# Optimization experiments

Hardware: AMD Instinct MI355X
Metric: run time of the kernel (lower is better)

Reference implementation:

```python
import math
import jax, jax.numpy as jnp
import numpy as np

H, N2, B, L = 256, 32, 8, 4096
DT_MIN, DT_MAX = 1e-3, 1e-1

def setup_inputs() -> dict:
    key = jax.random.key(0)
    ks = jax.random.split(key, 6)
    u = jax.random.normal(ks[0], (B, H, L), dtype=jnp.float32)
    # log_dt uniform in [log(dt_min), log(dt_max)] as in S4DKernel.__init__
    log_dt = jax.random.uniform(ks[1], (H,), dtype=jnp.float32) * (
        math.log(DT_MAX) - math.log(DT_MIN)) + math.log(DT_MIN)
    C = jax.random.normal(ks[2], (H, N2, 2), dtype=jnp.float32)  # view_as_real of complex C
    log_A_real = jnp.log(0.5 * jnp.ones((H, N2), dtype=jnp.float32))
    A_imag = math.pi * jnp.broadcast_to(jnp.arange(N2, dtype=jnp.float32), (H, N2))
    D = jax.random.normal(ks[3], (H,), dtype=jnp.float32)
    W = jax.random.normal(ks[4], (2 * H, H), dtype=jnp.float32) / math.sqrt(H)
    b = jax.random.normal(ks[5], (2 * H,), dtype=jnp.float32) * 0.01
    return {"u": u, "log_dt": log_dt, "C": C, "log_A_real": log_A_real,
            "A_imag": A_imag, "D": D, "W": W, "b": b}

def reference(u, log_dt, C, log_A_real, A_imag, D, W, b):
    # ---- S4DKernel: generate convolution kernel k (H, L) ----
    Lk = u.shape[-1]
    dt = jnp.exp(log_dt)                                  # (H,)
    Cc = C[..., 0] + 1j * C[..., 1]                       # (H, N2) complex
    A = -jnp.exp(log_A_real) + 1j * A_imag                # (H, N2) complex
    dtA = A * dt[:, None]                                 # (H, N2)
    # Vandermonde: exp(dtA * l) for l in [0, L)  -> (H, N2, L) complex
    K = jnp.exp(dtA[:, :, None] * jnp.arange(Lk, dtype=jnp.float32))
    Ct = Cc * (jnp.exp(dtA) - 1.0) / A                    # (H, N2)
    k = 2.0 * jnp.einsum('hn,hnl->hl', Ct, K).real        # (H, L) float32
    # ---- FFT long convolution ----
    n = 2 * Lk
    k_f = jnp.fft.rfft(k, n=n)                            # (H, n//2+1)
    u_f = jnp.fft.rfft(u, n=n)                            # (B, H, n//2+1)
    y = jnp.fft.irfft(u_f * k_f, n=n)[..., :Lk]           # (B, H, L)
    y = y + u * D[:, None]                                # skip connection
    y = jax.nn.gelu(y, approximate=False)                 # nn.GELU (exact)
    # ---- output 1x1 conv (H -> 2H) + GLU over channel dim ----
    z = jnp.einsum('oh,bhl->bol', W, y) + b[None, :, None]  # (B, 2H, L)
    a, g = jnp.split(z, 2, axis=1)
    return a * jax.nn.sigmoid(g)                          # (B, H, L)
```

## Files before the change

### kernel.cpp

```cpp
#include <hip/hip_runtime.h>
#include <math.h>

#define H 256
#define N2 32
#define Bsz 8
#define Lseq 4096
#define BH (Bsz*H)
#define NCH 32
#define LC (Lseq/NCH)
#define HN (H*N2)

#define S_OFF  0
#define Y_OFF  (S_OFF + BH*NCH*N2*2)
#define WB_OFF (Y_OFF + (BH*Lseq/2))
#define KB_OFF (WB_OFF + (512*256/2))
#define EB_OFF (KB_OFF + (H*128/2))
#define VB_OFF (EB_OFF + (H*128*64/2))

typedef __attribute__((ext_vector_type(8))) short bf16x8;
typedef __attribute__((ext_vector_type(8))) unsigned short u16x8;
typedef __attribute__((ext_vector_type(4))) float f32x4;

__device__ __forceinline__ unsigned short f2bf(float x) {
  union { float f; unsigned int u; } v; v.f = x;
  unsigned int r = v.u + 0x7fffu + ((v.u >> 16) & 1u);
  return (unsigned short)(r >> 16);
}
__device__ __forceinline__ unsigned int packbf(float lo, float hi) {
  return (unsigned int)f2bf(lo) | ((unsigned int)f2bf(hi) << 16);
}

__global__ __launch_bounds__(128) void k_prep(const float* __restrict__ log_dt,
                                              const float* __restrict__ C,
                                              const float* __restrict__ lar,
                                              const float* __restrict__ aim,
                                              const float* __restrict__ W,
                                              unsigned short* __restrict__ Wb,
                                              unsigned short* __restrict__ kb,
                                              unsigned short* __restrict__ Eb,
                                              unsigned short* __restrict__ Vb) {
  int h = blockIdx.x;
  int j = threadIdx.x;
  {
    int i = h * 128 + j;
    float4 v = *(const float4*)&W[i * 4];
    uint2 p; p.x = packbf(v.x, v.y); p.y = packbf(v.z, v.w);
    *(uint2*)&Wb[i * 4] = p;
  }
  float dt = expf(log_dt[h]);
  float kacc = 0.f;
  unsigned short* Erow = Eb + (h * 128 + j) * 64;
  for (int n = 0; n < 32; n++) {
    int hn = (h << 5) + n;
    float Ar = -expf(lar[hn]), Ai = aim[hn];
    float dAr = Ar * dt, dAi = Ai * dt;
    float er = expf(dAr), sw, cw;
    sincosf(dAi, &sw, &cw);
    float wr = er * cw, wi = er * sw;
    float emr = wr - 1.f, emi = wi;
    float inv = 1.f / (Ar * Ar + Ai * Ai);
    float qr = (emr * Ar + emi * Ai) * inv;
    float qi = (emi * Ar - emr * Ai) * inv;
    float Cr = C[2 * hn], Ci = C[2 * hn + 1];
    float c2r = 2.f * (Cr * qr - Ci * qi);
    float c2i = 2.f * (Cr * qi + Ci * qr);
    float ej = expf(dAr * (float)j), sj, cj;
    sincosf(dAi * (float)j, &sj, &cj);
    kacc = fmaf(c2r, ej * cj, fmaf(-c2i, ej * sj, kacc));
    float e1 = expf(dAr * (float)(j + 1)), s1, c1;
    sincosf(dAi * (float)(j + 1), &s1, &c1);
    float w1r = e1 * c1, w1i = e1 * s1;
    Erow[2 * n]     = f2bf(c2r * w1r - c2i * w1i);
    Erow[2 * n + 1] = f2bf(-(c2r * w1i + c2i * w1r));
    float ev = expf(dAr * (float)(127 - j)), sv, cv;
    sincosf(dAi * (float)(127 - j), &sv, &cv);
    Vb[(h * 64 + 2 * n) * 128 + j]     = f2bf(ev * cv);
    Vb[(h * 64 + 2 * n + 1) * 128 + j] = f2bf(ev * sv);
  }
  kb[h * 128 + j] = f2bf(kacc);
}

__global__ __launch_bounds__(256) void k_state(const float* __restrict__ u,
                                               const unsigned short* __restrict__ Vb,
                                               float* __restrict__ S) {
  __shared__ unsigned short Ul[64][136];
  __shared__ unsigned short Bl[64][136];
  int h   = blockIdx.x;
  int mq  = blockIdx.y;
  int tid = threadIdx.x;
  int wv = tid >> 6, lane = tid & 63;
  int n16 = lane & 15, quad = lane >> 4;
  int m0 = wv * 16;
  f32x4 acc[4] = {};
#pragma unroll
  for (int i = 0; i < 8; i++) {
    int e = tid + i * 256;
    int r = e >> 5, c4 = e & 31;
    int b = mq * 2 + (r >> 5), c = r & 31;
    float4 v = *(const float4*)&u[((b * 256 + h) * 4096 + c * 128 + c4 * 4)];
    *(unsigned int*)&Ul[r][c4 * 4]     = packbf(v.x, v.y);
    *(unsigned int*)&Ul[r][c4 * 4 + 2] = packbf(v.z, v.w);
  }
#pragma unroll
  for (int i = 0; i < 4; i++) {
    int e = tid + i * 256;
    int p = e >> 4, s8 = e & 15;
    *(u16x8*)&Bl[p][s8 * 8] = *(const u16x8*)&Vb[(h * 64 + p) * 128 + s8 * 8];
  }
  __syncthreads();
#pragma unroll
  for (int ks = 0; ks < 128; ks += 32) {
    int kc = ks + quad * 8;
    bf16x8 af = *(const bf16x8*)&Ul[m0 + n16][kc];
#pragma unroll
    for (int nt = 0; nt < 4; nt++) {
      bf16x8 bf = *(const bf16x8*)&Bl[nt * 16 + n16][kc];
      acc[nt] = __builtin_amdgcn_mfma_f32_16x16x32_bf16(af, bf, acc[nt], 0, 0, 0);
    }
  }
#pragma unroll
  for (int reg = 0; reg < 4; reg++) {
    int m = m0 + quad * 4 + reg;
    int b = mq * 2 + (m >> 5), c = m & 31;
#pragma unroll
    for (int nt = 0; nt < 4; nt++) {
      int p = nt * 16 + n16;
      S[((b * 256 + h) * 32 + c) * 64 + p] = acc[nt][reg];
    }
  }
}

__global__ void k_prefix(const float* __restrict__ log_dt, const float* __restrict__ lar,
                         const float* __restrict__ aim, float* __restrict__ S) {
  int t = blockIdx.x * blockDim.x + threadIdx.x;
  if (t >= BH * N2) return;
  int n = t & 31, bh = t >> 5;
  int h = bh & (H - 1);
  int hn = (h << 5) + n;
  float dt  = expf(log_dt[h]);
  float dAr = -expf(lar[hn]) * dt, dAi = aim[hn] * dt;
  float eL = expf(dAr * (float)LC), sL, cL;
  sincosf(dAi * (float)LC, &sL, &cL);
  float wLr = eL * cL, wLi = eL * sL;
  float fr = 0.f, fi = 0.f;
  for (int c = 0; c < NCH; c++) {
    int si = (((bh * NCH + c) << 5) + n) << 1;
    float sr = S[si], s1 = S[si + 1];
    S[si] = fr; S[si + 1] = fi;
    float nr = fmaf(wLr, fr, fmaf(-wLi, fi, sr));
    float ni = fmaf(wLr, fi, fmaf(wLi, fr, s1));
    fr = nr; fi = ni;
  }
}

__global__ __launch_bounds__(256) void k_emit(const float* __restrict__ u,
                                              const float* __restrict__ S,
                                              const unsigned short* __restrict__ kb,
                                              const unsigned short* __restrict__ Eb,
                                              const float* __restrict__ Dp,
                                              unsigned short* __restrict__ yb) {
  __shared__ unsigned short Ul[64][72];
  __shared__ unsigned short Bl[128][72];
  __shared__ unsigned short kbuf[128];
  int h   = blockIdx.x;
  int mq  = blockIdx.y;
  int tid = threadIdx.x;
  int wv = tid >> 6, lane = tid & 63;
  int n16 = lane & 15, quad = lane >> 4;
  int m0 = wv * 16;
  f32x4 acc[8] = {};

  if (tid < 128) kbuf[tid] = kb[h * 128 + tid];

  for (int ks = 0; ks < 128; ks += 64) {
    __syncthreads();
#pragma unroll
    for (int i = 0; i < 4; i++) {
      int e = tid + i * 256;
      int r = e >> 4, c4 = e & 15;
      int b = mq * 2 + (r >> 5), c = r & 31;
      const float* up = u + ((b * 256 + h) * 4096 + c * 128 + ks + c4 * 4);
      float4 v = *(const float4*)up;
      *(unsigned int*)&Ul[r][c4 * 4]     = packbf(v.x, v.y);
      *(unsigned int*)&Ul[r][c4 * 4 + 2] = packbf(v.z, v.w);
    }
#pragma unroll
    for (int i = 0; i < 32; i++) {
      int e = tid + i * 256;
      int jj = e >> 6, m = e & 63;
      int d = jj - ks - m;
      Bl[jj][m] = (d >= 0) ? kbuf[d] : (unsigned short)0;
    }
    __syncthreads();
#pragma unroll
    for (int ks2 = 0; ks2 < 64; ks2 += 32) {
      int kc = ks2 + quad * 8;
      bf16x8 af = *(const bf16x8*)&Ul[m0 + n16][kc];
#pragma unroll
      for (int nt = 0; nt < 8; nt++) {
        bf16x8 bf = *(const bf16x8*)&Bl[nt * 16 + n16][kc];
        acc[nt] = __builtin_amdgcn_mfma_f32_16x16x32_bf16(af, bf, acc[nt], 0, 0, 0);
      }
    }
  }

  __syncthreads();
#pragma unroll
  for (int i = 0; i < 4; i++) {
    int e = tid + i * 256;
    int r = e >> 4, c4 = e & 15;
    int b = mq * 2 + (r >> 5), c = r & 31;
    const float* sp = S + ((b * 256 + h) * 32 + c) * 64 + c4 * 4;
    float4 v = *(const float4*)sp;
    *(unsigned int*)&Ul[r][c4 * 4]     = packbf(v.x, v.y);
    *(unsigned int*)&Ul[r][c4 * 4 + 2] = packbf(v.z, v.w);
  }
#pragma unroll
  for (int i = 0; i < 4; i++) {
    int e = tid + i * 256;
    int jj = e >> 3, p8 = e & 7;
    *(u16x8*)&Bl[jj][p8 * 8] = *(const u16x8*)&Eb[(h * 128 + jj) * 64 + p8 * 8];
  }
  __syncthreads();
#pragma unroll
  for (int ks2 = 0; ks2 < 64; ks2 += 32) {
    int kc = ks2 + quad * 8;
    bf16x8 af = *(const bf16x8*)&Ul[m0 + n16][kc];
#pragma unroll
    for (int nt = 0; nt < 8; nt++) {
      bf16x8 bf = *(const bf16x8*)&Bl[nt * 16 + n16][kc];
      acc[nt] = __builtin_amdgcn_mfma_f32_16x16x32_bf16(af, bf, acc[nt], 0, 0, 0);
    }
  }

  float Dh = Dp[h];
#pragma unroll
  for (int reg = 0; reg < 4; reg++) {
    int m = m0 + quad * 4 + reg;
    int b = mq * 2 + (m >> 5), c = m & 31;
    int base = (b * 256 + h) * 4096 + c * 128;
#pragma unroll
    for (int nt = 0; nt < 8; nt++) {
      int j = nt * 16 + n16;
      float uv = u[base + j];
      float v  = fmaf(Dh, uv, acc[nt][reg]);
      float ge = 0.5f * v * (1.0f + erff(v * 0.70710678118654752f));
      yb[base + j] = f2bf(ge);
    }
  }
}

__global__ __launch_bounds__(256) void k_gemm(const unsigned short* __restrict__ yb,
                                              const unsigned short* __restrict__ Wb,
                                              const float* __restrict__ bias,
                                              float* __restrict__ out) {
  __shared__ unsigned short Ws[128][72];
  __shared__ unsigned short Ys[128][72];
  int tid  = threadIdx.x;
  int l0   = blockIdx.x * 128;
  int o0   = blockIdx.y * 64;
  int bb   = blockIdx.z;
  int wave = tid >> 6;
  int lane = tid & 63;
  int wo   = wave & 1;
  int wl   = wave >> 1;
  int n    = lane & 15;
  int quad = lane >> 4;

  f32x4 acc_a[2][4] = {};
  f32x4 acc_g[2][4] = {};

  for (int kk = 0; kk < H; kk += 64) {
#pragma unroll
    for (int i = 0; i < 4; i++) {
      int e = tid + i * 256;
      int r = e >> 3, s = e & 7;
      int gr = (r < 64) ? (o0 + r) : (192 + o0 + r);
      *(u16x8*)&Ws[r][s * 8] = *(const u16x8*)&Wb[gr * 256 + kk + s * 8];
    }
    {
      int kcol = tid & 63;
      int lg0  = tid >> 6;
      const unsigned short* yrow = yb + (bb * 256 + kk + kcol) * 4096 + l0;
#pragma unroll
      for (int i = 0; i < 4; i++) {
        int l8 = (lg0 * 4 + i) * 8;
        u16x8 v = *(const u16x8*)&yrow[l8];
#pragma unroll
        for (int jj = 0; jj < 8; jj++)
          Ys[l8 + jj][kcol] = v[jj];
      }
    }
    __syncthreads();
#pragma unroll
    for (int ks = 0; ks < 64; ks += 32) {
      int kc = ks + quad * 8;
      bf16x8 af_a[2], af_g[2], bfr[4];
#pragma unroll
      for (int mt = 0; mt < 2; mt++) {
        af_a[mt] = *(const bf16x8*)&Ws[wo * 32 + mt * 16 + n][kc];
        af_g[mt] = *(const bf16x8*)&Ws[64 + wo * 32 + mt * 16 + n][kc];
      }
#pragma unroll
      for (int lt = 0; lt < 4; lt++)
        bfr[lt] = *(const bf16x8*)&Ys[wl * 64 + lt * 16 + n][kc];
#pragma unroll
      for (int mt = 0; mt < 2; mt++)
#pragma unroll
        for (int lt = 0; lt < 4; lt++) {
          acc_a[mt][lt] = __builtin_amdgcn_mfma_f32_16x16x32_bf16(af_a[mt], bfr[lt], acc_a[mt][lt], 0, 0, 0);
          acc_g[mt][lt] = __builtin_amdgcn_mfma_f32_16x16x32_bf16(af_g[mt], bfr[lt], acc_g[mt][lt], 0, 0, 0);
        }
    }
    __syncthreads();
  }
#pragma unroll
  for (int mt = 0; mt < 2; mt++) {
    int ob = o0 + wo * 32 + mt * 16 + quad * 4;
#pragma unroll
    for (int reg = 0; reg < 4; reg++) {
      int op = ob + reg;
      float ba = bias[op], bg = bias[H + op];
      float* orow = &out[(bb * H + op) * Lseq + l0 + wl * 64 + n];
#pragma unroll
      for (int lt = 0; lt < 4; lt++) {
        float a = acc_a[mt][lt][reg] + ba;
        float g = acc_g[mt][lt][reg] + bg;
        orow[lt * 16] = a / (1.0f + expf(-g));
      }
    }
  }
}

extern "C" void kernel_launch(void* const* d_in, const int* in_sizes, int n_in,
                              void* d_out, int out_size, void* d_ws, size_t ws_size,
                              hipStream_t stream) {
  const float* u      = (const float*)d_in[0];
  const float* log_dt = (const float*)d_in[1];
  const float* C      = (const float*)d_in[2];
  const float* lar    = (const float*)d_in[3];
  const float* aim    = (const float*)d_in[4];
  const float* Dp     = (const float*)d_in[5];
  const float* W      = (const float*)d_in[6];
  const float* bias   = (const float*)d_in[7];
  float* out = (float*)d_out;
  float* ws  = (float*)d_ws;
  float* S   = ws + S_OFF;
  unsigned short* yb  = (unsigned short*)(ws + Y_OFF);
  unsigned short* Wb  = (unsigned short*)(ws + WB_OFF);
  unsigned short* kbg = (unsigned short*)(ws + KB_OFF);
  unsigned short* Ebg = (unsigned short*)(ws + EB_OFF);
  unsigned short* Vbg = (unsigned short*)(ws + VB_OFF);

  hipLaunchKernelGGL(k_prep,   dim3(H), dim3(128), 0, stream, log_dt, C, lar, aim, W, Wb, kbg, Ebg, Vbg);
  hipLaunchKernelGGL(k_state,  dim3(H, 4), dim3(256), 0, stream, u, Vbg, S);
  hipLaunchKernelGGL(k_prefix, dim3(BH * N2 / 256), dim3(256), 0, stream, log_dt, lar, aim, S);
  hipLaunchKernelGGL(k_emit,   dim3(H, 4), dim3(256), 0, stream, u, S, kbg, Ebg, Dp, yb);
  hipLaunchKernelGGL(k_gemm,   dim3(Lseq / 128, H / 64, Bsz), dim3(256), 0, stream, yb, Wb, bias, out);
}
```

Before: 174.8 us.

## Precompute Toeplitz kernel tiles in prep and fuse emit into single K=192 pass

The 128x128 lower-triangular Toeplitz block of the convolution kernel is now built once per channel in k_prep and stored in the workspace, instead of being rebuilt in shared memory by every k_emit block. k_emit loads the full u chunk, the chunk states and the Toeplitz/E tiles into one shared buffer and runs a single MFMA loop over K=192, removing two barrier phases. The skip term now reads the bf16 u from shared memory instead of re-reading fp32 u from global, which slightly lowers precision. In exchange the workspace grows by an H*128*128 bf16 Toeplitz array, and k_emit uses more shared memory per block, which may reduce occupancy.

```diff
diff --git a/kernel.cpp b/kernel.cpp
--- a/kernel.cpp
+++ b/kernel.cpp
@@ -13,8 +13,8 @@
 #define S_OFF  0
 #define Y_OFF  (S_OFF + BH*NCH*N2*2)
 #define WB_OFF (Y_OFF + (BH*Lseq/2))
-#define KB_OFF (WB_OFF + (512*256/2))
-#define EB_OFF (KB_OFF + (H*128/2))
+#define TB_OFF (WB_OFF + (512*256/2))
+#define EB_OFF (TB_OFF + (H*128*128/2))
 #define VB_OFF (EB_OFF + (H*128*64/2))
 
 typedef __attribute__((ext_vector_type(8))) short bf16x8;
@@ -28,6 +28,10 @@
 }
 __device__ __forceinline__ unsigned int packbf(float lo, float hi) {
   return (unsigned int)f2bf(lo) | ((unsigned int)f2bf(hi) << 16);
+}
+__device__ __forceinline__ float bf2f(unsigned short b) {
+  union { unsigned int u; float f; } v; v.u = ((unsigned int)b) << 16;
+  return v.f;
 }
 
 __global__ __launch_bounds__(128) void k_prep(const float* __restrict__ log_dt,
@@ -36,9 +40,10 @@
                                               const float* __restrict__ aim,
                                               const float* __restrict__ W,
                                               unsigned short* __restrict__ Wb,
-                                              unsigned short* __restrict__ kb,
+                                              unsigned short* __restrict__ Tb,
                                               unsigned short* __restrict__ Eb,
                                               unsigned short* __restrict__ Vb) {
+  __shared__ unsigned short kbuf[128];
   int h = blockIdx.x;
   int j = threadIdx.x;
   {
@@ -77,7 +82,19 @@
     Vb[(h * 64 + 2 * n) * 128 + j]     = f2bf(ev * cv);
     Vb[(h * 64 + 2 * n + 1) * 128 + j] = f2bf(ev * sv);
   }
-  kb[h * 128 + j] = f2bf(kacc);
+  kbuf[j] = f2bf(kacc);
+  __syncthreads();
+  unsigned short* Trow = Tb + (h * 128 + j) * 128;
+#pragma unroll
+  for (int s8 = 0; s8 < 16; s8++) {
+    u16x8 v;
+#pragma unroll
+    for (int t = 0; t < 8; t++) {
+      int m = s8 * 8 + t;
+      v[t] = (j >= m) ? kbuf[j - m] : (unsigned short)0;
+    }
+    *(u16x8*)&Trow[s8 * 8] = v;
+  }
 }
 
 __global__ __launch_bounds__(256) void k_state(const float* __restrict__ u,
@@ -155,13 +172,12 @@
 
 __global__ __launch_bounds__(256) void k_emit(const float* __restrict__ u,
                                               const float* __restrict__ S,
-                                              const unsigned short* __restrict__ kb,
+                                              const unsigned short* __restrict__ Tb,
                                               const unsigned short* __restrict__ Eb,
                                               const float* __restrict__ Dp,
                                               unsigned short* __restrict__ yb) {
-  __shared__ unsigned short Ul[64][72];
-  __shared__ unsigned short Bl[128][72];
-  __shared__ unsigned short kbuf[128];
+  __shared__ unsigned short Ul[64][200];
+  __shared__ unsigned short Bl[128][200];
   int h   = blockIdx.x;
   int mq  = blockIdx.y;
   int tid = threadIdx.x;
@@ -170,61 +186,40 @@
   int m0 = wv * 16;
   f32x4 acc[8] = {};
 
-  if (tid < 128) kbuf[tid] = kb[h * 128 + tid];
-
-  for (int ks = 0; ks < 128; ks += 64) {
-    __syncthreads();
-#pragma unroll
-    for (int i = 0; i < 4; i++) {
-      int e = tid + i * 256;
-      int r = e >> 4, c4 = e & 15;
-      int b = mq * 2 + (r >> 5), c = r & 31;
-      const float* up = u + ((b * 256 + h) * 4096 + c * 128 + ks + c4 * 4);
-      float4 v = *(const float4*)up;
-      *(unsigned int*)&Ul[r][c4 * 4]     = packbf(v.x, v.y);
-      *(unsigned int*)&Ul[r][c4 * 4 + 2] = packbf(v.z, v.w);
-    }
-#pragma unroll
-    for (int i = 0; i < 32; i++) {
-      int e = tid + i * 256;
-      int jj = e >> 6, m = e & 63;
-      int d = jj - ks - m;
-      Bl[jj][m] = (d >= 0) ? kbuf[d] : (unsigned short)0;
-    }
-    __syncthreads();
-#pragma unroll
-    for (int ks2 = 0; ks2 < 64; ks2 += 32) {
-      int kc = ks2 + quad * 8;
-      bf16x8 af = *(const bf16x8*)&Ul[m0 + n16][kc];
-#pragma unroll
-      for (int nt = 0; nt < 8; nt++) {
-        bf16x8 bf = *(const bf16x8*)&Bl[nt * 16 + n16][kc];
-        acc[nt] = __builtin_amdgcn_mfma_f32_16x16x32_bf16(af, bf, acc[nt], 0, 0, 0);
-      }
-    }
-  }
-
-  __syncthreads();
+#pragma unroll
+  for (int i = 0; i < 8; i++) {
+    int e = tid + i * 256;
+    int r = e >> 5, c4 = e & 31;
+    int b = mq * 2 + (r >> 5), c = r & 31;
+    float4 v = *(const float4*)&u[((b * 256 + h) * 4096 + c * 128 + c4 * 4)];
+    *(unsigned int*)&Ul[r][c4 * 4]     = packbf(v.x, v.y);
+    *(unsigned int*)&Ul[r][c4 * 4 + 2] = packbf(v.z, v.w);
+  }
 #pragma unroll
   for (int i = 0; i < 4; i++) {
     int e = tid + i * 256;
     int r = e >> 4, c4 = e & 15;
     int b = mq * 2 + (r >> 5), c = r & 31;
-    const float* sp = S + ((b * 256 + h) * 32 + c) * 64 + c4 * 4;
-    float4 v = *(const float4*)sp;
-    *(unsigned int*)&Ul[r][c4 * 4]     = packbf(v.x, v.y);
-    *(unsigned int*)&Ul[r][c4 * 4 + 2] = packbf(v.z, v.w);
+    float4 v = *(const float4*)&S[((b * 256 + h) * 32 + c) * 64 + c4 * 4];
+    *(unsigned int*)&Ul[r][128 + c4 * 4]     = packbf(v.x, v.y);
+    *(unsigned int*)&Ul[r][128 + c4 * 4 + 2] = packbf(v.z, v.w);
+  }
+#pragma unroll
+  for (int i = 0; i < 8; i++) {
+    int e = tid + i * 256;
+    int jj = e >> 4, s8 = e & 15;
+    *(u16x8*)&Bl[jj][s8 * 8] = *(const u16x8*)&Tb[(h * 128 + jj) * 128 + s8 * 8];
   }
 #pragma unroll
   for (int i = 0; i < 4; i++) {
     int e = tid + i * 256;
     int jj = e >> 3, p8 = e & 7;
-    *(u16x8*)&Bl[jj][p8 * 8] = *(const u16x8*)&Eb[(h * 128 + jj) * 64 + p8 * 8];
+    *(u16x8*)&Bl[jj][128 + p8 * 8] = *(const u16x8*)&Eb[(h * 128 + jj) * 64 + p8 * 8];
   }
   __syncthreads();
 #pragma unroll
-  for (int ks2 = 0; ks2 < 64; ks2 += 32) {
-    int kc = ks2 + quad * 8;
+  for (int ks = 0; ks < 192; ks += 32) {
+    int kc = ks + quad * 8;
     bf16x8 af = *(const bf16x8*)&Ul[m0 + n16][kc];
 #pragma unroll
     for (int nt = 0; nt < 8; nt++) {
@@ -232,7 +227,6 @@
       acc[nt] = __builtin_amdgcn_mfma_f32_16x16x32_bf16(af, bf, acc[nt], 0, 0, 0);
     }
   }
-
   float Dh = Dp[h];
 #pragma unroll
   for (int reg = 0; reg < 4; reg++) {
@@ -242,7 +236,7 @@
 #pragma unroll
     for (int nt = 0; nt < 8; nt++) {
       int j = nt * 16 + n16;
-      float uv = u[base + j];
+      float uv = bf2f(Ul[m][j]);
       float v  = fmaf(Dh, uv, acc[nt][reg]);
       float ge = 0.5f * v * (1.0f + erff(v * 0.70710678118654752f));
       yb[base + j] = f2bf(ge);
@@ -348,13 +342,13 @@
   float* S   = ws + S_OFF;
   unsigned short* yb  = (unsigned short*)(ws + Y_OFF);
   unsigned short* Wb  = (unsigned short*)(ws + WB_OFF);
-  unsigned short* kbg = (unsigned short*)(ws + KB_OFF);
+  unsigned short* Tbg = (unsigned short*)(ws + TB_OFF);
   unsigned short* Ebg = (unsigned short*)(ws + EB_OFF);
   unsigned short* Vbg = (unsigned short*)(ws + VB_OFF);
 
-  hipLaunchKernelGGL(k_prep,   dim3(H), dim3(128), 0, stream, log_dt, C, lar, aim, W, Wb, kbg, Ebg, Vbg);
+  hipLaunchKernelGGL(k_prep,   dim3(H), dim3(128), 0, stream, log_dt, C, lar, aim, W, Wb, Tbg, Ebg, Vbg);
   hipLaunchKernelGGL(k_state,  dim3(H, 4), dim3(256), 0, stream, u, Vbg, S);
   hipLaunchKernelGGL(k_prefix, dim3(BH * N2 / 256), dim3(256), 0, stream, log_dt, lar, aim, S);
-  hipLaunchKernelGGL(k_emit,   dim3(H, 4), dim3(256), 0, stream, u, S, kbg, Ebg, Dp, yb);
+  hipLaunchKernelGGL(k_emit,   dim3(H, 4), dim3(256), 0, stream, u, S, Tbg, Ebg, Dp, yb);
   hipLaunchKernelGGL(k_gemm,   dim3(Lseq / 128, H / 64, Bsz), dim3(256), 0, stream, yb, Wb, bias, out);
 }
```

New measurement: 178.5 us. +2.1%, slower.
